# Kernel tuning notes

Hardware: AMD Instinct MI355X
Metric: run time of the kernel (lower is better)

The kernel has to match this reference:

```python
import jax, jax.numpy as jnp
import numpy as np

KERNEL = 3  # 2*half_size + 1 with half_size=1
ITER = 20


def _pool(v):
    # MaxPool2d(kernel=3, stride=1, padding=1) == SAME max reduce_window on NCHW
    return jax.lax.reduce_window(v, -jnp.inf, jax.lax.max,
                                 (1, 1, KERNEL, KERNEL), (1, 1, 1, 1), 'SAME')


def _erode(v):
    return -_pool(-v)


def setup_inputs() -> dict:
    key = jax.random.key(0)
    x = jax.random.normal(key, (16, 1, 1024, 1024), dtype=jnp.float32)
    return {"x": x}


def reference(x):
    skel0 = x - _pool(_erode(x))  # open(x) = dilate(erode(x))

    def step(carry, _):
        xc, skel = carry
        xc = _erode(xc)
        skel = skel + (xc - _pool(_erode(xc)))
        return (xc, skel), None

    (_, skel), _ = jax.lax.scan(step, (x, skel0), None, length=ITER)
    return skel
```

## Files before the change

kernel.cpp:

```cpp
#include <hip/hip_runtime.h>


static constexpr int W = 1024, H = 1024, NIMG = 16;
static constexpr int RCH = 32;
static constexpr int NSTEP = RCH + 16;
static constexpr int WPB = 4;
static constexpr float BIG = 3.0e38f;

__device__ __forceinline__ float min3f(float a, float b, float c) { return fminf(fminf(a, b), c); }
__device__ __forceinline__ float max3f(float a, float b, float c) { return fmaxf(fmaxf(a, b), c); }

__device__ __forceinline__ float dpp_left(float v) {
    return __int_as_float(__builtin_amdgcn_mov_dpp(__float_as_int(v), 0x138, 0xF, 0xF, true));
}
__device__ __forceinline__ float dpp_right(float v) {
    return __int_as_float(__builtin_amdgcn_mov_dpp(__float_as_int(v), 0x130, 0xF, 0xF, true));
}

template<bool FIRST, bool WRITE_E, bool EDGE, int PFI>
__device__ __forceinline__
void pipe_step(int t, int y0, int gx,
               bool leftEdge, bool rightEdge, bool lane_ok,
               const float* __restrict__ in, float* __restrict__ eo,
               float* __restrict__ sk,
               float4 (&OB)[7], float4 (&MB)[7], float4& OD, float4& MD,
               float4 (&acc)[8], float4 (&pf)[2], float4 (&skpf)[2])
{
    float4 cur;
    if (!EDGE || (unsigned)t < (unsigned)H) cur = pf[PFI];
    else                                    cur = make_float4(BIG, BIG, BIG, BIG);
    {
        const int nr = t + 2;
        if ((!EDGE || (unsigned)nr < (unsigned)H) && nr <= y0 + RCH + 7)
            pf[PFI] = *(const float4*)&in[(size_t)nr * W + gx];
    }

#pragma unroll
    for (int s = 0; s < 7; ++s) {
        const float4 fOld = OB[s];
        const float4 fMid = MB[s];

        float4 vm;
        vm.x = min3f(fOld.x, fMid.x, cur.x);
        vm.y = min3f(fOld.y, fMid.y, cur.y);
        vm.z = min3f(fOld.z, fMid.z, cur.z);
        vm.w = min3f(fOld.w, fMid.w, cur.w);
        float lft = dpp_left(vm.w);
        float rgt = dpp_right(vm.x);
        if (leftEdge)  lft = BIG;
        if (rightEdge) rgt = BIG;
        float4 en;
        en.x = min3f(lft,  vm.x, vm.y);
        en.y = min3f(vm.x, vm.y, vm.z);
        en.z = min3f(vm.y, vm.z, vm.w);
        en.w = min3f(vm.z, vm.w, rgt);

        OB[s] = cur;

        float4 gOld, gMid;
        if (s < 6) { gOld = OB[s + 1]; gMid = MB[s + 1]; }
        else       { gOld = OD;        gMid = MD;        }
        const bool topOK = !EDGE || ((t - s - 3) >= 0);
        const bool botOK = !EDGE || ((t - s - 1) < H);
        float4 vx;
        {
            float txx = topOK ? gOld.x : -BIG, bxx = botOK ? en.x : -BIG;
            float txy = topOK ? gOld.y : -BIG, bxy = botOK ? en.y : -BIG;
            float txz = topOK ? gOld.z : -BIG, bxz = botOK ? en.z : -BIG;
            float txw = topOK ? gOld.w : -BIG, bxw = botOK ? en.w : -BIG;
            vx.x = max3f(txx, gMid.x, bxx);
            vx.y = max3f(txy, gMid.y, bxy);
            vx.z = max3f(txz, gMid.z, bxz);
            vx.w = max3f(txw, gMid.w, bxw);
        }
        float dl = dpp_left(vx.w);
        float dr = dpp_right(vx.x);
        if (leftEdge)  dl = -BIG;
        if (rightEdge) dr = -BIG;
        float4 dn;
        dn.x = max3f(dl,   vx.x, vx.y);
        dn.y = max3f(vx.x, vx.y, vx.z);
        dn.z = max3f(vx.y, vx.z, vx.w);
        dn.w = max3f(vx.z, vx.w, dr);

        acc[6 - s].x += fOld.x - dn.x;
        acc[6 - s].y += fOld.y - dn.y;
        acc[6 - s].z += fOld.z - dn.z;
        acc[6 - s].w += fOld.w - dn.w;

        if (s == 6) {
            if (WRITE_E) {
                const int er = t - 7;
                if (er >= y0 && er < y0 + RCH && lane_ok)
                    *(float4*)&eo[(size_t)er * W + gx] = en;
            }
            OD = en;
        }
        cur = en;
    }

    if (t >= y0 + 8) {
        const int r = t - 8;
        float4 v = acc[0];
        if (!FIRST) {
            const float4 o = skpf[PFI];
            v.x += o.x; v.y += o.y; v.z += o.z; v.w += o.w;
        }
        if (lane_ok)
            *(float4*)&sk[(size_t)r * W + gx] = v;
    }
#pragma unroll
    for (int j = 0; j < 7; ++j) acc[j] = acc[j + 1];
    acc[7] = make_float4(0.f, 0.f, 0.f, 0.f);

    if (!FIRST) {
        const int pr = t - 6;
        if (pr >= y0 && pr < y0 + RCH)
            skpf[PFI] = *(const float4*)&sk[(size_t)pr * W + gx];
    }
}

template<bool FIRST, bool WRITE_E, bool EDGE>
__device__ __forceinline__
void sweep(int y0, int gx,
           bool leftEdge, bool rightEdge, bool lane_ok,
           const float* __restrict__ in, float* __restrict__ eo,
           float* __restrict__ sk)
{
    float4 B0[7], B1[7], D0, D1, acc[8], pf[2], skpf[2];
    const float4 big4 = make_float4(BIG, BIG, BIG, BIG);
    const float4 z4   = make_float4(0.f, 0.f, 0.f, 0.f);
#pragma unroll
    for (int s = 0; s < 7; ++s) { B0[s] = big4; B1[s] = big4; }
    D0 = big4; D1 = big4;
#pragma unroll
    for (int j = 0; j < 8; ++j) acc[j] = z4;
    pf[0] = big4; pf[1] = big4; skpf[0] = z4; skpf[1] = z4;

    {
        const int r0 = y0 - 8, r1 = y0 - 7;
        if (!EDGE || r0 >= 0) pf[0] = *(const float4*)&in[(size_t)r0 * W + gx];
        if (!EDGE || r1 >= 0) pf[1] = *(const float4*)&in[(size_t)r1 * W + gx];
    }

    const int t0 = y0 - 8;
#pragma unroll 1
    for (int t = t0; t < t0 + NSTEP; t += 2) {
        pipe_step<FIRST, WRITE_E, EDGE, 0>(t,     y0, gx, leftEdge, rightEdge, lane_ok,
                                           in, eo, sk, B0, B1, D0, D1, acc, pf, skpf);
        pipe_step<FIRST, WRITE_E, EDGE, 1>(t + 1, y0, gx, leftEdge, rightEdge, lane_ok,
                                           in, eo, sk, B1, B0, D1, D0, acc, pf, skpf);
    }
}

template<bool FIRST, bool WRITE_E>
__global__ __launch_bounds__(WPB * 64)
void skel_pipe(const float* __restrict__ ein, float* __restrict__ eout,
               float* __restrict__ skel)
{
    const int lane = threadIdx.x;
    const int bx = blockIdx.x;
    const int y0 = (blockIdx.y * WPB + (int)threadIdx.y) * RCH;
    const int img = blockIdx.z;
    const int x0 = (bx == 4) ? 768 : bx * 240;
    const int gx = x0 + 4 * lane;

    const size_t base = (size_t)img * (size_t)(W * H);
    const float* __restrict__ in = ein + base;
    float* __restrict__ eo = eout + base;
    float* __restrict__ sk = skel + base;

    const bool leftEdge  = (gx == 0);
    const bool rightEdge = (gx + 4 == W);
    const int own_lo = (bx == 0) ? 0 : ((bx == 4) ? 968 : x0 + 8);
    const int own_hi = (bx == 4) ? W : x0 + 248;
    const bool lane_ok = (gx >= own_lo) && (gx < own_hi);

    if (y0 >= 32 && y0 <= H - RCH - 32)
        sweep<FIRST, WRITE_E, false>(y0, gx, leftEdge, rightEdge, lane_ok, in, eo, sk);
    else
        sweep<FIRST, WRITE_E, true >(y0, gx, leftEdge, rightEdge, lane_ok, in, eo, sk);
}

extern "C" void kernel_launch(void* const* d_in, const int* in_sizes, int n_in,
                              void* d_out, int out_size, void* d_ws, size_t ws_size,
                              hipStream_t stream)
{
    const float* x = (const float*)d_in[0];
    float* skel = (float*)d_out;
    const size_t n = (size_t)NIMG * W * H;

    float* e0 = (float*)d_ws;
    float* e1 = e0 + n;

    dim3 grid(5, H / (RCH * WPB), NIMG);
    dim3 block(64, WPB);

    skel_pipe<true,  true ><<<grid, block, 0, stream>>>(x,  e0, skel);
    skel_pipe<false, true ><<<grid, block, 0, stream>>>(e0, e1, skel);
    skel_pipe<false, false><<<grid, block, 0, stream>>>(e1, e0, skel);
}
```

Measured before the change: 324.1 us.

## Unroll pipeline by eight with rotating accumulator ring and edge-specialized sweeps

The sweep loop is unrolled by eight so the accumulator array becomes a compile-time rotating ring indexed by phase, which removes the per-step shift of eight float4 registers and the zeroing. Left and right image-edge checks are made template parameters, so interior column blocks compile without the edge selects. The grid axes are also swapped so consecutive blocks walk row chunks instead of column blocks, which changes memory access locality. The cost is more code size and more template instantiations, which may add instruction-cache and register pressure.

```diff
diff --git a/kernel.cpp b/kernel.cpp
--- a/kernel.cpp
+++ b/kernel.cpp
@@ -17,7 +17,7 @@
     return __int_as_float(__builtin_amdgcn_mov_dpp(__float_as_int(v), 0x130, 0xF, 0xF, true));
 }
 
-template<bool FIRST, bool WRITE_E, bool EDGE, int PFI>
+template<bool FIRST, bool WRITE_E, bool EDGE, bool LE, bool RE, int PHASE>
 __device__ __forceinline__
 void pipe_step(int t, int y0, int gx,
                bool leftEdge, bool rightEdge, bool lane_ok,
@@ -26,6 +26,8 @@
                float4 (&OB)[7], float4 (&MB)[7], float4& OD, float4& MD,
                float4 (&acc)[8], float4 (&pf)[2], float4 (&skpf)[2])
 {
+    constexpr int PFI = PHASE & 1;
+
     float4 cur;
     if (!EDGE || (unsigned)t < (unsigned)H) cur = pf[PFI];
     else                                    cur = make_float4(BIG, BIG, BIG, BIG);
@@ -47,8 +49,8 @@
         vm.w = min3f(fOld.w, fMid.w, cur.w);
         float lft = dpp_left(vm.w);
         float rgt = dpp_right(vm.x);
-        if (leftEdge)  lft = BIG;
-        if (rightEdge) rgt = BIG;
+        if (LE && leftEdge)  lft = BIG;
+        if (RE && rightEdge) rgt = BIG;
         float4 en;
         en.x = min3f(lft,  vm.x, vm.y);
         en.y = min3f(vm.x, vm.y, vm.z);
@@ -75,18 +77,28 @@
         }
         float dl = dpp_left(vx.w);
         float dr = dpp_right(vx.x);
-        if (leftEdge)  dl = -BIG;
-        if (rightEdge) dr = -BIG;
+        if (LE && leftEdge)  dl = -BIG;
+        if (RE && rightEdge) dr = -BIG;
         float4 dn;
         dn.x = max3f(dl,   vx.x, vx.y);
         dn.y = max3f(vx.x, vx.y, vx.z);
         dn.z = max3f(vx.y, vx.z, vx.w);
         dn.w = max3f(vx.z, vx.w, dr);
 
-        acc[6 - s].x += fOld.x - dn.x;
-        acc[6 - s].y += fOld.y - dn.y;
-        acc[6 - s].z += fOld.z - dn.z;
-        acc[6 - s].w += fOld.w - dn.w;
+        constexpr int SL_BASE = 0;
+        const int slot = (PHASE + 6 - s) & 7;
+        (void)SL_BASE;
+        if (s == 0) {
+            acc[slot].x = fOld.x - dn.x;
+            acc[slot].y = fOld.y - dn.y;
+            acc[slot].z = fOld.z - dn.z;
+            acc[slot].w = fOld.w - dn.w;
+        } else {
+            acc[slot].x += fOld.x - dn.x;
+            acc[slot].y += fOld.y - dn.y;
+            acc[slot].z += fOld.z - dn.z;
+            acc[slot].w += fOld.w - dn.w;
+        }
 
         if (s == 6) {
             if (WRITE_E) {
@@ -101,7 +113,7 @@
 
     if (t >= y0 + 8) {
         const int r = t - 8;
-        float4 v = acc[0];
+        float4 v = acc[PHASE];
         if (!FIRST) {
             const float4 o = skpf[PFI];
             v.x += o.x; v.y += o.y; v.z += o.z; v.w += o.w;
@@ -109,9 +121,6 @@
         if (lane_ok)
             *(float4*)&sk[(size_t)r * W + gx] = v;
     }
-#pragma unroll
-    for (int j = 0; j < 7; ++j) acc[j] = acc[j + 1];
-    acc[7] = make_float4(0.f, 0.f, 0.f, 0.f);
 
     if (!FIRST) {
         const int pr = t - 6;
@@ -120,7 +129,7 @@
     }
 }
 
-template<bool FIRST, bool WRITE_E, bool EDGE>
+template<bool FIRST, bool WRITE_E, bool EDGE, bool LE, bool RE>
 __device__ __forceinline__
 void sweep(int y0, int gx,
            bool leftEdge, bool rightEdge, bool lane_ok,
@@ -145,11 +154,23 @@
 
     const int t0 = y0 - 8;
 #pragma unroll 1
-    for (int t = t0; t < t0 + NSTEP; t += 2) {
-        pipe_step<FIRST, WRITE_E, EDGE, 0>(t,     y0, gx, leftEdge, rightEdge, lane_ok,
-                                           in, eo, sk, B0, B1, D0, D1, acc, pf, skpf);
-        pipe_step<FIRST, WRITE_E, EDGE, 1>(t + 1, y0, gx, leftEdge, rightEdge, lane_ok,
-                                           in, eo, sk, B1, B0, D1, D0, acc, pf, skpf);
+    for (int t = t0; t < t0 + NSTEP; t += 8) {
+        pipe_step<FIRST, WRITE_E, EDGE, LE, RE, 0>(t,     y0, gx, leftEdge, rightEdge, lane_ok,
+                                                   in, eo, sk, B0, B1, D0, D1, acc, pf, skpf);
+        pipe_step<FIRST, WRITE_E, EDGE, LE, RE, 1>(t + 1, y0, gx, leftEdge, rightEdge, lane_ok,
+                                                   in, eo, sk, B1, B0, D1, D0, acc, pf, skpf);
+        pipe_step<FIRST, WRITE_E, EDGE, LE, RE, 2>(t + 2, y0, gx, leftEdge, rightEdge, lane_ok,
+                                                   in, eo, sk, B0, B1, D0, D1, acc, pf, skpf);
+        pipe_step<FIRST, WRITE_E, EDGE, LE, RE, 3>(t + 3, y0, gx, leftEdge, rightEdge, lane_ok,
+                                                   in, eo, sk, B1, B0, D1, D0, acc, pf, skpf);
+        pipe_step<FIRST, WRITE_E, EDGE, LE, RE, 4>(t + 4, y0, gx, leftEdge, rightEdge, lane_ok,
+                                                   in, eo, sk, B0, B1, D0, D1, acc, pf, skpf);
+        pipe_step<FIRST, WRITE_E, EDGE, LE, RE, 5>(t + 5, y0, gx, leftEdge, rightEdge, lane_ok,
+                                                   in, eo, sk, B1, B0, D1, D0, acc, pf, skpf);
+        pipe_step<FIRST, WRITE_E, EDGE, LE, RE, 6>(t + 6, y0, gx, leftEdge, rightEdge, lane_ok,
+                                                   in, eo, sk, B0, B1, D0, D1, acc, pf, skpf);
+        pipe_step<FIRST, WRITE_E, EDGE, LE, RE, 7>(t + 7, y0, gx, leftEdge, rightEdge, lane_ok,
+                                                   in, eo, sk, B1, B0, D1, D0, acc, pf, skpf);
     }
 }
 
@@ -159,8 +180,8 @@
                float* __restrict__ skel)
 {
     const int lane = threadIdx.x;
-    const int bx = blockIdx.x;
-    const int y0 = (blockIdx.y * WPB + (int)threadIdx.y) * RCH;
+    const int bx = blockIdx.y;
+    const int y0 = (blockIdx.x * WPB + (int)threadIdx.y) * RCH;
     const int img = blockIdx.z;
     const int x0 = (bx == 4) ? 768 : bx * 240;
     const int gx = x0 + 4 * lane;
@@ -176,10 +197,18 @@
     const int own_hi = (bx == 4) ? W : x0 + 248;
     const bool lane_ok = (gx >= own_lo) && (gx < own_hi);
 
-    if (y0 >= 32 && y0 <= H - RCH - 32)
-        sweep<FIRST, WRITE_E, false>(y0, gx, leftEdge, rightEdge, lane_ok, in, eo, sk);
-    else
-        sweep<FIRST, WRITE_E, true >(y0, gx, leftEdge, rightEdge, lane_ok, in, eo, sk);
+    const bool edge_chunk = !(y0 >= 32 && y0 <= H - RCH - 32);
+
+    if (bx == 0) {
+        if (edge_chunk) sweep<FIRST, WRITE_E, true,  true,  false>(y0, gx, leftEdge, rightEdge, lane_ok, in, eo, sk);
+        else            sweep<FIRST, WRITE_E, false, true,  false>(y0, gx, leftEdge, rightEdge, lane_ok, in, eo, sk);
+    } else if (bx == 4) {
+        if (edge_chunk) sweep<FIRST, WRITE_E, true,  false, true >(y0, gx, leftEdge, rightEdge, lane_ok, in, eo, sk);
+        else            sweep<FIRST, WRITE_E, false, false, true >(y0, gx, leftEdge, rightEdge, lane_ok, in, eo, sk);
+    } else {
+        if (edge_chunk) sweep<FIRST, WRITE_E, true,  false, false>(y0, gx, leftEdge, rightEdge, lane_ok, in, eo, sk);
+        else            sweep<FIRST, WRITE_E, false, false, false>(y0, gx, leftEdge, rightEdge, lane_ok, in, eo, sk);
+    }
 }
 
 extern "C" void kernel_launch(void* const* d_in, const int* in_sizes, int n_in,
@@ -193,7 +222,7 @@
     float* e0 = (float*)d_ws;
     float* e1 = e0 + n;
 
-    dim3 grid(5, H / (RCH * WPB), NIMG);
+    dim3 grid(H / (RCH * WPB), 5, NIMG);
     dim3 block(64, WPB);
 
     skel_pipe<true,  true ><<<grid, block, 0, stream>>>(x,  e0, skel);
```

Result: slower. 407.6 us (+25.8%).
